# Kernel optimization log

Measured on AMD Instinct MI355X. Metric: run time of the kernel, lower is better.

Reference implementation:

```python
import jax, jax.numpy as jnp
import numpy as np

N_NODES = 50000
N_EDGES = 800000
F_IN = 512
H1 = 64
H2 = 128
N_CLASSES = 10
N_GRAPHS = 64


def _sage_conv(x, src, dst, w_l, b_l, w_r, n_nodes):
    # mean-aggregate neighbor features (messages flow src -> dst), then
    # out = lin_l(mean_neigh) + lin_r(x)   (PyG SAGEConv defaults)
    msg = x[src]                                           # [E, F] gather
    agg = jax.ops.segment_sum(msg, dst, num_segments=n_nodes)
    deg = jax.ops.segment_sum(jnp.ones((src.shape[0], 1), x.dtype), dst,
                              num_segments=n_nodes)
    mean = agg / jnp.maximum(deg, 1.0)                     # 0 for isolated nodes
    return mean @ w_l + b_l + x @ w_r


def setup_inputs() -> dict:
    key = jax.random.key(0)
    ks = jax.random.split(key, 12)
    x = jax.random.normal(ks[0], (N_NODES, F_IN), dtype=jnp.float32)
    edge_index = jax.random.randint(ks[1], (2, N_EDGES), 0, N_NODES, dtype=jnp.int64)
    batch = jnp.sort(jax.random.randint(ks[2], (N_NODES,), 0, N_GRAPHS, dtype=jnp.int64))

    def glorot(k, fan_in, fan_out):
        s = jnp.sqrt(6.0 / (fan_in + fan_out)).astype(jnp.float32)
        return jax.random.uniform(k, (fan_in, fan_out), jnp.float32, -s, s)

    return {
        "x": x, "edge_index": edge_index, "batch": batch,
        "w1_l": glorot(ks[3], F_IN, H1), "b1_l": jnp.zeros((H1,), jnp.float32),
        "w1_r": glorot(ks[4], F_IN, H1),
        "w2_l": glorot(ks[5], H1, H2), "b2_l": jnp.zeros((H2,), jnp.float32),
        "w2_r": glorot(ks[6], H1, H2),
        "w_fc": glorot(ks[7], H2, N_CLASSES),
        "b_fc": jnp.zeros((N_CLASSES,), jnp.float32),
    }


def reference(x, edge_index, batch, w1_l, b1_l, w1_r, w2_l, b2_l, w2_r, w_fc, b_fc):
    src, dst = edge_index[0], edge_index[1]
    n = x.shape[0]
    h = jax.nn.relu(_sage_conv(x, src, dst, w1_l, b1_l, w1_r, n))
    # dropout is identity in eval mode
    h = _sage_conv(h, src, dst, w2_l, b2_l, w2_r, n)        # [N, H2]
    # global mean pool over graphs
    summed = jax.ops.segment_sum(h, batch, num_segments=N_GRAPHS)
    cnt = jax.ops.segment_sum(jnp.ones((n, 1), h.dtype), batch, num_segments=N_GRAPHS)
    pooled = summed / jnp.maximum(cnt, 1.0)                 # [G, H2]
    logits = pooled @ w_fc + b_fc                           # [G, C]
    return jax.nn.log_softmax(logits, axis=1)
```

## Files before the change

### kernel.cpp

```cpp
#include <hip/hip_runtime.h>

#define NN 50000
#define NE 800000
#define FIN 512
#define H1DIM 64
#define H2DIM 128
#define NC 10
#define NG 64

typedef __attribute__((ext_vector_type(8))) short bf16x8;
typedef __attribute__((ext_vector_type(4))) float f32x4;

__device__ inline short f2bf(float f) {
  unsigned u = __float_as_uint(f);
  unsigned r = u + 0x7fffu + ((u >> 16) & 1u);
  return (short)(r >> 16);
}
__device__ inline float bf2f(short s) {
  return __uint_as_float(((unsigned)(unsigned short)s) << 16);
}

__global__ __launch_bounds__(256) void wbt_prep_kernel(
    const float* __restrict__ wl, const float* __restrict__ wr,
    short* __restrict__ wbt) {
  int idx = blockIdx.x * 256 + threadIdx.x;
  int n = idx >> 9;
  int k = idx & 511;
  float v = (n < 64) ? wl[(size_t)k * 64 + n] : wr[(size_t)k * 64 + (n - 64)];
  wbt[idx] = f2bf(v);
}

__global__ __launch_bounds__(256) void gemm1_mfma_kernel(
    const float* __restrict__ x, const short* __restrict__ wbt,
    short* __restrict__ xwl, float* __restrict__ xwr) {
  __shared__ short Asl[64][40];
  __shared__ short Bsl[128][40];

  const int tid = threadIdx.x;
  const int wave = tid >> 6;
  const int lane = tid & 63;
  const int l15 = lane & 15;
  const int q = lane >> 4;
  const int mw = (wave & 1) * 32;
  const int nw = (wave >> 1) * 64;
  const int m0 = blockIdx.x * 64;

  const f32x4 z = {0.f, 0.f, 0.f, 0.f};
  f32x4 acc[2][4];
#pragma unroll
  for (int mi = 0; mi < 2; mi++)
#pragma unroll
    for (int ni = 0; ni < 4; ni++) acc[mi][ni] = z;

  const int ar = tid >> 2;
  const int ac = (tid & 3) * 8;
  const int agm = m0 + ar;
  const int bn = tid >> 1;
  const int bc = (tid & 1) * 16;

  for (int k0 = 0; k0 < FIN; k0 += 32) {
    float4 v0 = make_float4(0.f, 0.f, 0.f, 0.f);
    float4 v1 = make_float4(0.f, 0.f, 0.f, 0.f);
    if (agm < NN) {
      const float* p = x + (size_t)agm * FIN + k0 + ac;
      v0 = *(const float4*)(p);
      v1 = *(const float4*)(p + 4);
    }
    bf16x8 apack;
    apack[0] = f2bf(v0.x); apack[1] = f2bf(v0.y);
    apack[2] = f2bf(v0.z); apack[3] = f2bf(v0.w);
    apack[4] = f2bf(v1.x); apack[5] = f2bf(v1.y);
    apack[6] = f2bf(v1.z); apack[7] = f2bf(v1.w);
    *(bf16x8*)(&Asl[ar][ac]) = apack;
    const short* bp = wbt + (size_t)bn * FIN + k0 + bc;
    *(bf16x8*)(&Bsl[bn][bc]) = *(const bf16x8*)(bp);
    *(bf16x8*)(&Bsl[bn][bc + 8]) = *(const bf16x8*)(bp + 8);
    __syncthreads();

    bf16x8 afrag[2], bfrag[4];
#pragma unroll
    for (int mi = 0; mi < 2; mi++)
      afrag[mi] = *(const bf16x8*)(&Asl[mw + mi * 16 + l15][q * 8]);
#pragma unroll
    for (int ni = 0; ni < 4; ni++)
      bfrag[ni] = *(const bf16x8*)(&Bsl[nw + ni * 16 + l15][q * 8]);
#pragma unroll
    for (int mi = 0; mi < 2; mi++)
#pragma unroll
      for (int ni = 0; ni < 4; ni++)
        acc[mi][ni] = __builtin_amdgcn_mfma_f32_16x16x32_bf16(
            afrag[mi], bfrag[ni], acc[mi][ni], 0, 0, 0);
    __syncthreads();
  }

#pragma unroll
  for (int mi = 0; mi < 2; mi++) {
    int row_base = m0 + mw + mi * 16 + q * 4;
#pragma unroll
    for (int ni = 0; ni < 4; ni++) {
      int col = nw + ni * 16 + l15;
      int c = col & 63;
#pragma unroll
      for (int r = 0; r < 4; r++) {
        int row = row_base + r;
        if (row < NN) {
          if (col < 64) xwl[(size_t)row * 64 + c] = f2bf(acc[mi][ni][r]);
          else          xwr[(size_t)row * 64 + c] = acc[mi][ni][r];
        }
      }
    }
  }
}

__global__ __launch_bounds__(256) void hist_kernel(const int* __restrict__ dst,
                                                   int* __restrict__ cnt) {
  int e = blockIdx.x * 256 + threadIdx.x;
  if (e < NE) atomicAdd(&cnt[dst[e]], 1);
}

#define SCAN_BLOCKS 196

__global__ __launch_bounds__(256) void scan1_kernel(const int* __restrict__ cnt,
                                                    int* __restrict__ excl,
                                                    int* __restrict__ bsum) {
  __shared__ int s[256];
  int t = threadIdx.x;
  int i = blockIdx.x * 256 + t;
  int v = (i < NN) ? cnt[i] : 0;
  s[t] = v;
  __syncthreads();
  for (int off = 1; off < 256; off <<= 1) {
    int u = (t >= off) ? s[t - off] : 0;
    __syncthreads();
    s[t] += u;
    __syncthreads();
  }
  if (i < NN) excl[i] = s[t] - v;
  if (t == 255) bsum[blockIdx.x] = s[255];
}

__global__ __launch_bounds__(256) void scan2_kernel(int* __restrict__ bsum) {
  __shared__ int s[256];
  int t = threadIdx.x;
  int v = (t < SCAN_BLOCKS) ? bsum[t] : 0;
  s[t] = v;
  __syncthreads();
  for (int off = 1; off < 256; off <<= 1) {
    int u = (t >= off) ? s[t - off] : 0;
    __syncthreads();
    s[t] += u;
    __syncthreads();
  }
  bsum[t] = s[t] - v;
}

__global__ __launch_bounds__(256) void scan3_kernel(const int* __restrict__ bsum,
                                                    int* __restrict__ rowptr,
                                                    int* __restrict__ cursor) {
  int t = threadIdx.x;
  int i = blockIdx.x * 256 + t;
  if (i < NN) {
    int p = rowptr[i] + bsum[blockIdx.x];
    rowptr[i] = p;
    cursor[i] = p;
  }
  if (i == 0) rowptr[NN] = NE;
}

__global__ __launch_bounds__(256) void scatter_kernel(
    const int* __restrict__ src, const int* __restrict__ dst,
    int* __restrict__ cursor, int* __restrict__ ssrc) {
  int e = blockIdx.x * 256 + threadIdx.x;
  if (e < NE) {
    int p = atomicAdd(&cursor[dst[e]], 1);
    ssrc[p] = src[e];
  }
}

__global__ __launch_bounds__(256) void agg1_h1_kernel(
    const int* __restrict__ rowptr, const int* __restrict__ ssrc,
    const short* __restrict__ xwl, const float* __restrict__ xwr,
    const float* __restrict__ b1, short* __restrict__ h1) {
  int node = blockIdx.x * 4 + (threadIdx.x >> 6);
  if (node >= NN) return;
  int lane = threadIdx.x & 63;
  int c = lane & 7;
  int r = lane >> 3;
  int lo = rowptr[node], hi = rowptr[node + 1];
  float acc[8];
#pragma unroll
  for (int k = 0; k < 8; k++) acc[k] = 0.f;
  for (int e = lo + r; e < hi; e += 8) {
    int s = ssrc[e];
    bf16x8 v = *(const bf16x8*)(xwl + (size_t)s * 64 + c * 8);
#pragma unroll
    for (int k = 0; k < 8; k++) acc[k] += bf2f(v[k]);
  }
#pragma unroll
  for (int k = 0; k < 8; k++) {
    acc[k] += __shfl_xor(acc[k], 8);
    acc[k] += __shfl_xor(acc[k], 16);
    acc[k] += __shfl_xor(acc[k], 32);
  }
  if (r == 0) {
    float dg = fmaxf((float)(hi - lo), 1.0f);
    const float* xr = xwr + (size_t)node * 64 + c * 8;
    bf16x8 out;
#pragma unroll
    for (int k = 0; k < 8; k++) {
      float v = acc[k] / dg + b1[c * 8 + k] + xr[k];
      out[k] = f2bf(fmaxf(v, 0.f));
    }
    *(bf16x8*)(h1 + (size_t)node * 64 + c * 8) = out;
  }
}

__global__ __launch_bounds__(256) void agg2_kernel(
    const int* __restrict__ rowptr, const int* __restrict__ ssrc,
    const short* __restrict__ h1, float* __restrict__ agg2) {
  int node = blockIdx.x * 4 + (threadIdx.x >> 6);
  if (node >= NN) return;
  int lane = threadIdx.x & 63;
  int c = lane & 7;
  int r = lane >> 3;
  int lo = rowptr[node], hi = rowptr[node + 1];
  float acc[8];
#pragma unroll
  for (int k = 0; k < 8; k++) acc[k] = 0.f;
  for (int e = lo + r; e < hi; e += 8) {
    int s = ssrc[e];
    bf16x8 v = *(const bf16x8*)(h1 + (size_t)s * 64 + c * 8);
#pragma unroll
    for (int k = 0; k < 8; k++) acc[k] += bf2f(v[k]);
  }
#pragma unroll
  for (int k = 0; k < 8; k++) {
    acc[k] += __shfl_xor(acc[k], 8);
    acc[k] += __shfl_xor(acc[k], 16);
    acc[k] += __shfl_xor(acc[k], 32);
  }
  if (r == 0) {
    float* p = agg2 + (size_t)node * 64 + c * 8;
    f32x4 lo4 = {acc[0], acc[1], acc[2], acc[3]};
    f32x4 hi4 = {acc[4], acc[5], acc[6], acc[7]};
    *(f32x4*)(p) = lo4;
    *(f32x4*)(p + 4) = hi4;
  }
}

__global__ __launch_bounds__(256) void pool1_kernel(
    const int* __restrict__ batch, const float* __restrict__ agg2,
    const short* __restrict__ h1, const int* __restrict__ rowptr,
    float* __restrict__ poolA, float* __restrict__ poolB,
    float* __restrict__ poolCnt) {
  int t = threadIdx.x;
  int c = t & 15;
  int s = t >> 4;
  int n0 = blockIdx.x * 256 + s * 16;
  int n1 = n0 + 16;
  if (n1 > NN) n1 = NN;

  f32x4 aA = {0.f, 0.f, 0.f, 0.f};
  f32x4 aB = {0.f, 0.f, 0.f, 0.f};
  int cur_g = -1;
  float run = 0.f;
  for (int n = n0; n < n1; n++) {
    int g = batch[n];
    if (g != cur_g) {
      if (cur_g >= 0) {
        float* pa = poolA + (size_t)cur_g * 64 + c * 4;
        float* pb = poolB + (size_t)cur_g * 64 + c * 4;
#pragma unroll
        for (int k = 0; k < 4; k++) {
          atomicAdd(&pa[k], aA[k]);
          atomicAdd(&pb[k], aB[k]);
        }
        if (c == 0) atomicAdd(&poolCnt[cur_g], run);
      }
      cur_g = g;
      aA = (f32x4){0.f, 0.f, 0.f, 0.f};
      aB = (f32x4){0.f, 0.f, 0.f, 0.f};
      run = 0.f;
    }
    float rd = 1.0f / fmaxf((float)(rowptr[n + 1] - rowptr[n]), 1.0f);
    f32x4 a2 = *(const f32x4*)(agg2 + (size_t)n * 64 + c * 4);
    const short* hp = h1 + (size_t)n * 64 + c * 4;
#pragma unroll
    for (int k = 0; k < 4; k++) {
      aA[k] = fmaf(a2[k], rd, aA[k]);
      aB[k] += bf2f(hp[k]);
    }
    run += 1.f;
  }
  if (cur_g >= 0) {
    float* pa = poolA + (size_t)cur_g * 64 + c * 4;
    float* pb = poolB + (size_t)cur_g * 64 + c * 4;
#pragma unroll
    for (int k = 0; k < 4; k++) {
      atomicAdd(&pa[k], aA[k]);
      atomicAdd(&pb[k], aB[k]);
    }
    if (c == 0) atomicAdd(&poolCnt[cur_g], run);
  }
}

__global__ __launch_bounds__(128) void final_kernel(
    const float* __restrict__ poolA, const float* __restrict__ poolB,
    const float* __restrict__ poolCnt, const float* __restrict__ w2l,
    const float* __restrict__ w2r, const float* __restrict__ b2,
    const float* __restrict__ wfc, const float* __restrict__ bfc,
    float* __restrict__ out) {
  int g = blockIdx.x;
  int j = threadIdx.x;
  __shared__ float sp[H2DIM];
  __shared__ float sl[NC];

  float invc = 1.0f / fmaxf(poolCnt[g], 1.0f);
  float v = b2[j];
  for (int k = 0; k < 64; k++) {
    float a = poolA[g * 64 + k] * invc;
    float b = poolB[g * 64 + k] * invc;
    v = fmaf(a, w2l[k * 128 + j], v);
    v = fmaf(b, w2r[k * 128 + j], v);
  }
  sp[j] = v;
  __syncthreads();
  if (j < NC) {
    float lg = bfc[j];
    for (int k = 0; k < H2DIM; k++) lg = fmaf(sp[k], wfc[k * NC + j], lg);
    sl[j] = lg;
  }
  __syncthreads();
  if (j < NC) {
    float m = -1e30f;
    for (int k = 0; k < NC; k++) m = fmaxf(m, sl[k]);
    float s = 0.f;
    for (int k = 0; k < NC; k++) s += expf(sl[k] - m);
    out[g * NC + j] = sl[j] - m - logf(s);
  }
}

extern "C" void kernel_launch(void* const* d_in, const int* in_sizes, int n_in,
                              void* d_out, int out_size, void* d_ws,
                              size_t ws_size, hipStream_t stream) {
  const float* x   = (const float*)d_in[0];
  const int* edge  = (const int*)d_in[1];
  const int* batch = (const int*)d_in[2];
  const float* w1l = (const float*)d_in[3];
  const float* b1l = (const float*)d_in[4];
  const float* w1r = (const float*)d_in[5];
  const float* w2l = (const float*)d_in[6];
  const float* b2l = (const float*)d_in[7];
  const float* w2r = (const float*)d_in[8];
  const float* wfc = (const float*)d_in[9];
  const float* bfc = (const float*)d_in[10];
  float* out = (float*)d_out;

  const int* src = edge;
  const int* dst = edge + NE;

  const size_t NF = (size_t)NN * 64;
  int*   cnt     = (int*)d_ws;
  float* poolA   = (float*)(cnt + NN);
  float* poolB   = poolA + (size_t)NG * 64;
  float* poolCnt = poolB + (size_t)NG * 64;
  int*   cursor  = (int*)(poolCnt + NG);
  int*   rowptr  = cursor + NN;
  int*   ssrc    = rowptr + 50004;
  int*   bsum    = ssrc + NE;
  short* xwl     = (short*)(bsum + 256);
  short* h1s     = xwl + NF;
  float* xwr     = (float*)(h1s + NF);
  float* agg2    = xwr + NF;
  short* wbt     = (short*)(agg2 + NF);

  hipMemsetAsync(cnt, 0, (NN + 2 * NG * 64 + NG) * sizeof(int), stream);

  hist_kernel<<<(NE + 255) / 256, 256, 0, stream>>>(dst, cnt);
  scan1_kernel<<<SCAN_BLOCKS, 256, 0, stream>>>(cnt, rowptr, bsum);
  scan2_kernel<<<1, 256, 0, stream>>>(bsum);
  scan3_kernel<<<SCAN_BLOCKS, 256, 0, stream>>>(bsum, rowptr, cursor);
  scatter_kernel<<<(NE + 255) / 256, 256, 0, stream>>>(src, dst, cursor, ssrc);

  wbt_prep_kernel<<<65536 / 256, 256, 0, stream>>>(w1l, w1r, wbt);
  gemm1_mfma_kernel<<<(NN + 63) / 64, 256, 0, stream>>>(x, wbt, xwl, xwr);

  agg1_h1_kernel<<<(NN + 3) / 4, 256, 0, stream>>>(rowptr, ssrc, xwl, xwr, b1l, h1s);
  agg2_kernel<<<(NN + 3) / 4, 256, 0, stream>>>(rowptr, ssrc, h1s, agg2);
  pool1_kernel<<<SCAN_BLOCKS, 256, 0, stream>>>(batch, agg2, h1s, rowptr, poolA, poolB, poolCnt);
  final_kernel<<<NG, 128, 0, stream>>>(poolA, poolB, poolCnt, w2l, w2r, b2l, wfc, bfc, out);
}
```

Before: 372.4 us.

## Double-buffer GEMM1 shared tiles and vectorize histogram/scatter edge loads

The first-layer GEMM now uses two LDS buffers and prefetches the next K-slice of x and weights into registers while MFMAs run on the current slice, removing one barrier per iteration. Separately, the histogram and CSR-scatter kernels each process four edges per thread using int4 loads, cutting thread count and load instructions. The cost is doubled LDS use and more registers per thread in the GEMM. The atomics are unchanged.

```diff
diff --git a/kernel.cpp b/kernel.cpp
--- a/kernel.cpp
+++ b/kernel.cpp
@@ -33,8 +33,8 @@
 __global__ __launch_bounds__(256) void gemm1_mfma_kernel(
     const float* __restrict__ x, const short* __restrict__ wbt,
     short* __restrict__ xwl, float* __restrict__ xwr) {
-  __shared__ short Asl[64][40];
-  __shared__ short Bsl[128][40];
+  __shared__ short Asl[2][64][40];
+  __shared__ short Bsl[2][128][40];
 
   const int tid = threadIdx.x;
   const int wave = tid >> 6;
@@ -55,42 +55,75 @@
   const int ar = tid >> 2;
   const int ac = (tid & 3) * 8;
   const int agm = m0 + ar;
+  const bool arow_ok = (agm < NN);
   const int bn = tid >> 1;
   const int bc = (tid & 1) * 16;
 
-  for (int k0 = 0; k0 < FIN; k0 += 32) {
-    float4 v0 = make_float4(0.f, 0.f, 0.f, 0.f);
-    float4 v1 = make_float4(0.f, 0.f, 0.f, 0.f);
-    if (agm < NN) {
-      const float* p = x + (size_t)agm * FIN + k0 + ac;
-      v0 = *(const float4*)(p);
-      v1 = *(const float4*)(p + 4);
-    }
+  float4 av0 = make_float4(0.f, 0.f, 0.f, 0.f);
+  float4 av1 = make_float4(0.f, 0.f, 0.f, 0.f);
+  if (arow_ok) {
+    const float* p = x + (size_t)agm * FIN + ac;
+    av0 = *(const float4*)(p);
+    av1 = *(const float4*)(p + 4);
+  }
+  const short* bp0 = wbt + (size_t)bn * FIN + bc;
+  bf16x8 bv0 = *(const bf16x8*)(bp0);
+  bf16x8 bv1 = *(const bf16x8*)(bp0 + 8);
+  {
     bf16x8 apack;
-    apack[0] = f2bf(v0.x); apack[1] = f2bf(v0.y);
-    apack[2] = f2bf(v0.z); apack[3] = f2bf(v0.w);
-    apack[4] = f2bf(v1.x); apack[5] = f2bf(v1.y);
-    apack[6] = f2bf(v1.z); apack[7] = f2bf(v1.w);
-    *(bf16x8*)(&Asl[ar][ac]) = apack;
-    const short* bp = wbt + (size_t)bn * FIN + k0 + bc;
-    *(bf16x8*)(&Bsl[bn][bc]) = *(const bf16x8*)(bp);
-    *(bf16x8*)(&Bsl[bn][bc + 8]) = *(const bf16x8*)(bp + 8);
-    __syncthreads();
+    apack[0] = f2bf(av0.x); apack[1] = f2bf(av0.y);
+    apack[2] = f2bf(av0.z); apack[3] = f2bf(av0.w);
+    apack[4] = f2bf(av1.x); apack[5] = f2bf(av1.y);
+    apack[6] = f2bf(av1.z); apack[7] = f2bf(av1.w);
+    *(bf16x8*)(&Asl[0][ar][ac]) = apack;
+    *(bf16x8*)(&Bsl[0][bn][bc]) = bv0;
+    *(bf16x8*)(&Bsl[0][bn][bc + 8]) = bv1;
+  }
+  __syncthreads();
+
+  for (int ks = 0; ks < 16; ks++) {
+    const int cur = ks & 1;
+    const int nxt = cur ^ 1;
+    float4 nv0, nv1;
+    bf16x8 nb0, nb1;
+    if (ks < 15) {
+      int k0 = (ks + 1) * 32;
+      if (arow_ok) {
+        const float* p = x + (size_t)agm * FIN + k0 + ac;
+        nv0 = *(const float4*)(p);
+        nv1 = *(const float4*)(p + 4);
+      }
+      const short* bp = wbt + (size_t)bn * FIN + k0 + bc;
+      nb0 = *(const bf16x8*)(bp);
+      nb1 = *(const bf16x8*)(bp + 8);
+    }
 
     bf16x8 afrag[2], bfrag[4];
 #pragma unroll
     for (int mi = 0; mi < 2; mi++)
-      afrag[mi] = *(const bf16x8*)(&Asl[mw + mi * 16 + l15][q * 8]);
+      afrag[mi] = *(const bf16x8*)(&Asl[cur][mw + mi * 16 + l15][q * 8]);
 #pragma unroll
     for (int ni = 0; ni < 4; ni++)
-      bfrag[ni] = *(const bf16x8*)(&Bsl[nw + ni * 16 + l15][q * 8]);
+      bfrag[ni] = *(const bf16x8*)(&Bsl[cur][nw + ni * 16 + l15][q * 8]);
 #pragma unroll
     for (int mi = 0; mi < 2; mi++)
 #pragma unroll
       for (int ni = 0; ni < 4; ni++)
         acc[mi][ni] = __builtin_amdgcn_mfma_f32_16x16x32_bf16(
             afrag[mi], bfrag[ni], acc[mi][ni], 0, 0, 0);
-    __syncthreads();
+
+    if (ks < 15) {
+      bf16x8 apack;
+      if (!arow_ok) { nv0 = make_float4(0.f,0.f,0.f,0.f); nv1 = nv0; }
+      apack[0] = f2bf(nv0.x); apack[1] = f2bf(nv0.y);
+      apack[2] = f2bf(nv0.z); apack[3] = f2bf(nv0.w);
+      apack[4] = f2bf(nv1.x); apack[5] = f2bf(nv1.y);
+      apack[6] = f2bf(nv1.z); apack[7] = f2bf(nv1.w);
+      *(bf16x8*)(&Asl[nxt][ar][ac]) = apack;
+      *(bf16x8*)(&Bsl[nxt][bn][bc]) = nb0;
+      *(bf16x8*)(&Bsl[nxt][bn][bc + 8]) = nb1;
+      __syncthreads();
+    }
   }
 
 #pragma unroll
@@ -114,8 +147,14 @@
 
 __global__ __launch_bounds__(256) void hist_kernel(const int* __restrict__ dst,
                                                    int* __restrict__ cnt) {
-  int e = blockIdx.x * 256 + threadIdx.x;
-  if (e < NE) atomicAdd(&cnt[dst[e]], 1);
+  int i = (blockIdx.x * 256 + threadIdx.x) * 4;
+  if (i < NE) {
+    int4 d = *(const int4*)(dst + i);
+    atomicAdd(&cnt[d.x], 1);
+    atomicAdd(&cnt[d.y], 1);
+    atomicAdd(&cnt[d.z], 1);
+    atomicAdd(&cnt[d.w], 1);
+  }
 }
 
 #define SCAN_BLOCKS 196
@@ -170,10 +209,14 @@
 __global__ __launch_bounds__(256) void scatter_kernel(
     const int* __restrict__ src, const int* __restrict__ dst,
     int* __restrict__ cursor, int* __restrict__ ssrc) {
-  int e = blockIdx.x * 256 + threadIdx.x;
-  if (e < NE) {
-    int p = atomicAdd(&cursor[dst[e]], 1);
-    ssrc[p] = src[e];
+  int i = (blockIdx.x * 256 + threadIdx.x) * 4;
+  if (i < NE) {
+    int4 s = *(const int4*)(src + i);
+    int4 d = *(const int4*)(dst + i);
+    int p0 = atomicAdd(&cursor[d.x], 1); ssrc[p0] = s.x;
+    int p1 = atomicAdd(&cursor[d.y], 1); ssrc[p1] = s.y;
+    int p2 = atomicAdd(&cursor[d.z], 1); ssrc[p2] = s.z;
+    int p3 = atomicAdd(&cursor[d.w], 1); ssrc[p3] = s.w;
   }
 }
 
@@ -376,11 +419,11 @@
 
   hipMemsetAsync(cnt, 0, (NN + 2 * NG * 64 + NG) * sizeof(int), stream);
 
-  hist_kernel<<<(NE + 255) / 256, 256, 0, stream>>>(dst, cnt);
+  hist_kernel<<<(NE / 4 + 255) / 256, 256, 0, stream>>>(dst, cnt);
   scan1_kernel<<<SCAN_BLOCKS, 256, 0, stream>>>(cnt, rowptr, bsum);
   scan2_kernel<<<1, 256, 0, stream>>>(bsum);
   scan3_kernel<<<SCAN_BLOCKS, 256, 0, stream>>>(bsum, rowptr, cursor);
-  scatter_kernel<<<(NE + 255) / 256, 256, 0, stream>>>(src, dst, cursor, ssrc);
+  scatter_kernel<<<(NE / 4 + 255) / 256, 256, 0, stream>>>(src, dst, cursor, ssrc);
 
   wbt_prep_kernel<<<65536 / 256, 256, 0, stream>>>(w1l, w1r, wbt);
   gemm1_mfma_kernel<<<(NN + 63) / 64, 256, 0, stream>>>(x, wbt, xwl, xwr);
```

Result: no change. 374.4 us (+0.5%).
